# Kernel optimization log

Hardware: AMD Instinct MI355X
Metric: run time of the kernel (lower is better)

The kernel has to match this reference:

```python
import jax, jax.numpy as jnp
import numpy as np

B, C, H, W_SP = 1024, 256, 8, 8
HID = 512


def setup_inputs() -> dict:
    key = jax.random.key(0)
    ks = jax.random.split(key, 7)
    s_in = 1.0 / np.sqrt(C)
    s_hid = 1.0 / np.sqrt(HID)
    return {
        "anchor": jax.random.normal(ks[0], (B, C, H, W_SP), dtype=jnp.float32),
        "positive": jax.random.normal(ks[1], (B, C, H, W_SP), dtype=jnp.float32),
        "W1": jax.random.uniform(ks[2], (HID, C), minval=-s_in, maxval=s_in, dtype=jnp.float32),
        "b1": jax.random.uniform(ks[3], (HID,), minval=-s_in, maxval=s_in, dtype=jnp.float32),
        "W2": jax.random.uniform(ks[4], (C, HID), minval=-s_hid, maxval=s_hid, dtype=jnp.float32),
        "b2": jax.random.uniform(ks[5], (C,), minval=-s_hid, maxval=s_hid, dtype=jnp.float32),
        "Ww": jax.random.uniform(ks[6], (C, C), minval=-s_in, maxval=s_in, dtype=jnp.float32),
    }


def reference(anchor, positive, W1, b1, W2, b2, Ww):
    b, c, h, w = anchor.shape
    # Flatten spatial dims: [h*w, b, c] (equivalent to iterating y then x)
    a = jnp.transpose(anchor, (2, 3, 0, 1)).reshape(h * w, b, c)
    p = jnp.transpose(positive, (2, 3, 0, 1)).reshape(h * w, b, c)
    # anchor_xy = anchor_xy + MLP(anchor_xy); MLP = Linear->ReLU->Linear
    hidden = jax.nn.relu(jnp.einsum('pbc,hc->pbh', a, W1) + b1)
    a = a + jnp.einsum('pbh,ch->pbc', hidden, W2) + b2
    # pred_xy = W(anchor_xy), no bias
    pred = jnp.einsum('pbc,dc->pbd', a, Ww)
    # logits[p] = pred[p] @ positive[p].T : [h*w, b, b]
    logits = jnp.einsum('pbd,pkd->pbk', pred, p)
    logits = logits - jnp.max(logits, axis=2, keepdims=True)
    return logits  # [h*w, b, b], stacked version of the original python list
```

## Files before the change

kernel.cpp:

```cpp
#include <hip/hip_runtime.h>

typedef unsigned short u16;
typedef short bf16x8 __attribute__((ext_vector_type(8)));
typedef float f32x4 __attribute__((ext_vector_type(4)));

__device__ inline u16 f2bf(float f) {
  unsigned u = __float_as_uint(f);
  u += 0x7fff + ((u >> 16) & 1);
  return (u16)(u >> 16);
}

__device__ inline void gl_lds16(const u16* g, u16* l) {
  __builtin_amdgcn_global_load_lds((const __attribute__((address_space(1))) void*)g,
                                   (__attribute__((address_space(3))) void*)l, 16, 0, 0);
}

__global__ __launch_bounds__(256) void prep_weights(const float* __restrict__ Ww,
                                                    const float* __restrict__ W2,
                                                    const float* __restrict__ b2,
                                                    const float* __restrict__ W1,
                                                    u16* __restrict__ W2p,
                                                    float* __restrict__ b2p,
                                                    u16* __restrict__ W1b,
                                                    u16* __restrict__ Wwb) {
  int g = blockIdx.x * 256 + threadIdx.x;
  W1b[g] = f2bf(W1[g]);
  if (g < 65536) Wwb[g] = f2bf(Ww[g]);
  int d = g >> 9, h = g & 511;
  float s = 0.f;
  for (int c = 0; c < 256; c++) s += Ww[d * 256 + c] * W2[c * 512 + h];
  W2p[g] = f2bf(s);
  if (g < 256) {
    float t = 0.f;
    for (int c = 0; c < 256; c++) t += Ww[g * 256 + c] * b2[c];
    b2p[g] = t;
  }
}

__global__ __launch_bounds__(256) void transpose_cvt2(const float* __restrict__ ina,
                                                      const float* __restrict__ inp,
                                                      u16* __restrict__ outa,
                                                      u16* __restrict__ outp_) {
  __shared__ u16 T[64 * 256];
  const float* in = blockIdx.y ? inp : ina;
  u16* outp = blockIdx.y ? outp_ : outa;
  const int b = blockIdx.x;
  const int tid = threadIdx.x;
  const f32x4* in4 = (const f32x4*)in + (size_t)b * 4096;

  #pragma unroll
  for (int i = 0; i < 16; i++) {
    int local = i * 256 + tid;
    int c = local >> 4;
    int p4 = (local & 15) << 2;
    f32x4 v = __builtin_nontemporal_load(&in4[local]);
    int cc = c >> 3, co = c & 7;
    #pragma unroll
    for (int k = 0; k < 4; k++) {
      int p = p4 + k;
      int chunk = p * 32 + (cc ^ ((p >> 2) & 15));
      T[chunk * 8 + co] = f2bf(v[k]);
    }
  }
  __syncthreads();

  u16* ob = outp + (size_t)b * 256;
  #pragma unroll
  for (int j = 0; j < 8; j++) {
    int idx = j * 256 + tid;
    int row = idx >> 5;
    int col16 = idx & 31;
    int chunk = row * 32 + (col16 ^ ((row >> 2) & 15));
    bf16x8 vv = *(const bf16x8*)&T[chunk * 8];
    *(bf16x8*)&ob[((size_t)row << 18) + col16 * 8] = vv;
  }
}

__global__ __launch_bounds__(256, 3)
void gemm_bt(const u16* __restrict__ A1, const u16* __restrict__ B1, int K1len,
             const u16* __restrict__ A2, const u16* __restrict__ B2, int K2len,
             const float* __restrict__ bias, u16* __restrict__ C, int N, int relu,
             int lognbx) {
  __shared__ u16 As[128 * 64];
  __shared__ u16 Bs[128 * 64];
  const int tid = threadIdx.x;
  const int lane = tid & 63;
  const int wave = tid >> 6;
  const int wm = wave & 1;
  const int wn = wave >> 1;
  const int i_d = blockIdx.y * gridDim.x + blockIdx.x;
  const int xcd = i_d & 7;
  const int slot = i_d >> 3;
  const int bx = slot & ((1 << lognbx) - 1);
  const int by = xcd * (gridDim.y >> 3) + (slot >> lognbx);
  const int m0 = by * 128;
  const int n0 = bx * 128;
  const int q = lane >> 4;
  const int l15 = lane & 15;

  f32x4 acc[4][4];
  #pragma unroll
  for (int i = 0; i < 4; i++)
    #pragma unroll
    for (int j = 0; j < 4; j++) acc[i][j] = (f32x4)(0.0f);

  for (int seg = 0; seg < 2; seg++) {
    const u16* A = seg ? A2 : A1;
    const u16* B = seg ? B2 : B1;
    const int K = seg ? K2len : K1len;
    const int nkt = K >> 6;
    for (int kt = 0; kt < nkt; kt++) {
      #pragma unroll
      for (int c = 0; c < 4; c++) {
        int chunk = c * 256 + tid;
        int row = chunk >> 3;
        int cg = (chunk & 7) ^ (row & 7);
        gl_lds16(A + (size_t)(m0 + row) * K + kt * 64 + cg * 8, &As[chunk * 8]);
        gl_lds16(B + (size_t)(n0 + row) * K + kt * 64 + cg * 8, &Bs[chunk * 8]);
      }
      __syncthreads();
      #pragma unroll
      for (int ks = 0; ks < 2; ks++) {
        bf16x8 af[4], bfr[4];
        #pragma unroll
        for (int i = 0; i < 4; i++) {
          int row = wm * 64 + i * 16 + l15;
          af[i] = *(const bf16x8*)&As[row * 64 + (((ks * 4 + q) ^ (row & 7)) * 8)];
        }
        #pragma unroll
        for (int j = 0; j < 4; j++) {
          int row = wn * 64 + j * 16 + l15;
          bfr[j] = *(const bf16x8*)&Bs[row * 64 + (((ks * 4 + q) ^ (row & 7)) * 8)];
        }
        #pragma unroll
        for (int i = 0; i < 4; i++)
          #pragma unroll
          for (int j = 0; j < 4; j++)
            acc[i][j] = __builtin_amdgcn_mfma_f32_16x16x32_bf16(af[i], bfr[j], acc[i][j], 0, 0, 0);
      }
      __syncthreads();
    }
  }

  float bv[4];
  #pragma unroll
  for (int j = 0; j < 4; j++) bv[j] = bias[n0 + wn * 64 + j * 16 + l15];

  #pragma unroll
  for (int i = 0; i < 4; i++) {
    #pragma unroll
    for (int r = 0; r < 4; r++) {
      int row = m0 + wm * 64 + i * 16 + q * 4 + r;
      u16* crow = C + (size_t)row * N + n0 + wn * 64 + l15;
      #pragma unroll
      for (int j = 0; j < 4; j++) {
        float v = acc[i][j][r] + bv[j];
        if (relu) v = fmaxf(v, 0.0f);
        crow[j * 16] = f2bf(v);
      }
    }
  }
}

__global__ __launch_bounds__(512, 2)
void logits_k(const u16* __restrict__ pred, const u16* __restrict__ post,
              float* __restrict__ out) {
  __shared__ u16 As[64 * 256];
  __shared__ float pmax[8][64];
  const int tid = threadIdx.x;
  const int lane = tid & 63;
  const int wave = tid >> 6;
  const int q = lane >> 4;
  const int l15 = lane & 15;
  const int L = blockIdx.y * 16 + blockIdx.x;
  const int p = (L & 7) + ((L >> 7) << 3);
  const int m0 = ((L >> 3) & 15) * 64;
  const u16* Ap = pred + (((size_t)p * 1024 + m0) << 8);
  const u16* Bp = post + ((size_t)p << 18);

  #pragma unroll
  for (int c = 0; c < 4; c++) {
    int chunk = c * 512 + tid;
    int row = chunk >> 5;
    int cg = (chunk & 31) ^ (row & 7);
    gl_lds16(Ap + row * 256 + cg * 8, &As[chunk * 8]);
  }

  f32x4 acc[4][8];
  #pragma unroll
  for (int i = 0; i < 4; i++)
    #pragma unroll
    for (int j = 0; j < 8; j++) acc[i][j] = (f32x4)(0.0f);

  __syncthreads();

  const int nbase = wave * 128;
  #pragma unroll
  for (int kt = 0; kt < 8; kt++) {
    bf16x8 bfr[8];
    #pragma unroll
    for (int j = 0; j < 8; j++) {
      int n = nbase + j * 16 + l15;
      bfr[j] = *(const bf16x8*)&Bp[(size_t)n * 256 + kt * 32 + q * 8];
    }
    bf16x8 afr[4];
    #pragma unroll
    for (int i = 0; i < 4; i++) {
      int row = i * 16 + l15;
      afr[i] = *(const bf16x8*)&As[row * 256 + ((((kt << 2) + q) ^ (row & 7)) * 8)];
    }
    #pragma unroll
    for (int i = 0; i < 4; i++)
      #pragma unroll
      for (int j = 0; j < 8; j++)
        acc[i][j] = __builtin_amdgcn_mfma_f32_16x16x32_bf16(afr[i], bfr[j], acc[i][j], 0, 0, 0);
  }

  float rm[4][4];
  #pragma unroll
  for (int i = 0; i < 4; i++)
    #pragma unroll
    for (int r = 0; r < 4; r++) {
      float m = acc[i][0][r];
      #pragma unroll
      for (int j = 1; j < 8; j++) m = fmaxf(m, acc[i][j][r]);
      m = fmaxf(m, __shfl_xor(m, 1, 64));
      m = fmaxf(m, __shfl_xor(m, 2, 64));
      m = fmaxf(m, __shfl_xor(m, 4, 64));
      m = fmaxf(m, __shfl_xor(m, 8, 64));
      rm[i][r] = m;
    }
  if (l15 == 0) {
    #pragma unroll
    for (int i = 0; i < 4; i++)
      #pragma unroll
      for (int r = 0; r < 4; r++) pmax[wave][i * 16 + q * 4 + r] = rm[i][r];
  }
  __syncthreads();
  #pragma unroll
  for (int i = 0; i < 4; i++)
    #pragma unroll
    for (int r = 0; r < 4; r++) {
      int row = i * 16 + q * 4 + r;
      float m = pmax[0][row];
      #pragma unroll
      for (int w = 1; w < 8; w++) m = fmaxf(m, pmax[w][row]);
      rm[i][r] = m;
    }

  float* ob = out + ((size_t)p << 20) + (size_t)m0 * 1024 + nbase + l15;
  #pragma unroll
  for (int i = 0; i < 4; i++)
    #pragma unroll
    for (int r = 0; r < 4; r++) {
      float* orow = ob + (size_t)(i * 16 + q * 4 + r) * 1024;
      #pragma unroll
      for (int j = 0; j < 8; j++)
        __builtin_nontemporal_store(acc[i][j][r] - rm[i][r], &orow[j * 16]);
    }
}


extern "C" void kernel_launch(void* const* d_in, const int* in_sizes, int n_in,
                              void* d_out, int out_size, void* d_ws, size_t ws_size,
                              hipStream_t stream) {
  const float* anchor   = (const float*)d_in[0];
  const float* positive = (const float*)d_in[1];
  const float* W1       = (const float*)d_in[2];
  const float* b1       = (const float*)d_in[3];
  const float* W2       = (const float*)d_in[4];
  const float* b2       = (const float*)d_in[5];
  const float* Ww       = (const float*)d_in[6];
  float* out = (float*)d_out;
  char* ws = (char*)d_ws;

  u16*   A_t    = (u16*)(ws + 0x00000000);
  u16*   Pos_t  = (u16*)(ws + 0x02000000);
  u16*   hidden = (u16*)(ws + 0x04000000);
  u16*   pred   = (u16*)(ws + 0x08000000);
  u16*   W1b    = (u16*)(ws + 0x0A000000);
  u16*   Wwb    = (u16*)(ws + 0x0A100000);
  u16*   W2pb   = (u16*)(ws + 0x0A200000);
  float* b2p    = (float*)(ws + 0x0A300000);

  prep_weights<<<512, 256, 0, stream>>>(Ww, W2, b2, W1, W2pb, b2p, W1b, Wwb);
  transpose_cvt2<<<dim3(1024, 2), 256, 0, stream>>>(anchor, positive, A_t, Pos_t);

  gemm_bt<<<dim3(4, 512), 256, 0, stream>>>(A_t, W1b, 256, nullptr, nullptr, 0,
                                            b1, hidden, 512, 1, 2);
  gemm_bt<<<dim3(2, 512), 256, 0, stream>>>(A_t, Wwb, 256, hidden, W2pb, 512,
                                            b2p, pred, 256, 0, 1);
  logits_k<<<dim3(16, 64), 512, 0, stream>>>(pred, Pos_t, out);
}
```

Before: 522.0 us.

## Triple-buffer GEMM K-loop with async LDS loads and merge prep kernels

Rewrites the bf16 GEMM main loop to use a 3-stage ring of 32-wide K tiles loaded with global_load_lds, using partial vmcnt waits and one barrier per iteration so global loads overlap the MFMA work. The two K segments are flattened into one tile sequence so the pipeline carries across the segment boundary. Separately, weight preparation and input transpose/convert are merged into a single launch to remove one kernel launch and let the two run side by side. The smaller K tiles halve the work per barrier, and the hand-written waitcnt counts depend on the exact number of outstanding loads.

```diff
diff --git a/kernel.cpp b/kernel.cpp
--- a/kernel.cpp
+++ b/kernel.cpp
@@ -15,37 +15,37 @@
                                    (__attribute__((address_space(3))) void*)l, 16, 0, 0);
 }
 
-__global__ __launch_bounds__(256) void prep_weights(const float* __restrict__ Ww,
-                                                    const float* __restrict__ W2,
-                                                    const float* __restrict__ b2,
-                                                    const float* __restrict__ W1,
-                                                    u16* __restrict__ W2p,
-                                                    float* __restrict__ b2p,
-                                                    u16* __restrict__ W1b,
-                                                    u16* __restrict__ Wwb) {
-  int g = blockIdx.x * 256 + threadIdx.x;
-  W1b[g] = f2bf(W1[g]);
-  if (g < 65536) Wwb[g] = f2bf(Ww[g]);
-  int d = g >> 9, h = g & 511;
-  float s = 0.f;
-  for (int c = 0; c < 256; c++) s += Ww[d * 256 + c] * W2[c * 512 + h];
-  W2p[g] = f2bf(s);
-  if (g < 256) {
-    float t = 0.f;
-    for (int c = 0; c < 256; c++) t += Ww[g * 256 + c] * b2[c];
-    b2p[g] = t;
-  }
-}
-
-__global__ __launch_bounds__(256) void transpose_cvt2(const float* __restrict__ ina,
-                                                      const float* __restrict__ inp,
-                                                      u16* __restrict__ outa,
-                                                      u16* __restrict__ outp_) {
+__global__ __launch_bounds__(256) void prep_all(const float* __restrict__ anchor,
+                                                const float* __restrict__ positive,
+                                                u16* __restrict__ A_t, u16* __restrict__ Pos_t,
+                                                const float* __restrict__ Ww,
+                                                const float* __restrict__ W2,
+                                                const float* __restrict__ b2,
+                                                const float* __restrict__ W1,
+                                                u16* __restrict__ W2p, float* __restrict__ b2p,
+                                                u16* __restrict__ W1b, u16* __restrict__ Wwb) {
   __shared__ u16 T[64 * 256];
-  const float* in = blockIdx.y ? inp : ina;
-  u16* outp = blockIdx.y ? outp_ : outa;
-  const int b = blockIdx.x;
   const int tid = threadIdx.x;
+
+  if (blockIdx.x >= 2048) {
+    int g = (blockIdx.x - 2048) * 256 + tid;
+    W1b[g] = f2bf(W1[g]);
+    if (g < 65536) Wwb[g] = f2bf(Ww[g]);
+    int d = g >> 9, h = g & 511;
+    float s = 0.f;
+    for (int c = 0; c < 256; c++) s += Ww[d * 256 + c] * W2[c * 512 + h];
+    W2p[g] = f2bf(s);
+    if (g < 256) {
+      float t = 0.f;
+      for (int c = 0; c < 256; c++) t += Ww[g * 256 + c] * b2[c];
+      b2p[g] = t;
+    }
+    return;
+  }
+
+  const float* in = (blockIdx.x & 1024) ? positive : anchor;
+  u16* outp = (blockIdx.x & 1024) ? Pos_t : A_t;
+  const int b = blockIdx.x & 1023;
   const f32x4* in4 = (const f32x4*)in + (size_t)b * 4096;
 
   #pragma unroll
@@ -77,12 +77,12 @@
 }
 
 __global__ __launch_bounds__(256, 3)
-void gemm_bt(const u16* __restrict__ A1, const u16* __restrict__ B1, int K1len,
-             const u16* __restrict__ A2, const u16* __restrict__ B2, int K2len,
+void gemm_bt(const u16* __restrict__ A1, const u16* __restrict__ B1, int nkt1, int K1,
+             const u16* __restrict__ A2, const u16* __restrict__ B2, int nkt2, int K2,
              const float* __restrict__ bias, u16* __restrict__ C, int N, int relu,
              int lognbx) {
-  __shared__ u16 As[128 * 64];
-  __shared__ u16 Bs[128 * 64];
+  __shared__ u16 As[3][128 * 32];
+  __shared__ u16 Bs[3][128 * 32];
   const int tid = threadIdx.x;
   const int lane = tid & 63;
   const int wave = tid >> 6;
@@ -97,6 +97,21 @@
   const int n0 = bx * 128;
   const int q = lane >> 4;
   const int l15 = lane & 15;
+  const int nkt = nkt1 + nkt2;
+
+  auto stageF = [&](int kt, int buf) {
+    const u16* A; const u16* B; int K, k0;
+    if (kt < nkt1) { A = A1; B = B1; K = K1; k0 = kt << 5; }
+    else           { A = A2; B = B2; K = K2; k0 = (kt - nkt1) << 5; }
+    #pragma unroll
+    for (int c = 0; c < 2; c++) {
+      int chunk = c * 256 + tid;
+      int row = chunk >> 2;
+      int cg = (chunk & 3) ^ (row & 3);
+      gl_lds16(A + (size_t)(m0 + row) * K + k0 + cg * 8, &As[buf][chunk * 8]);
+      gl_lds16(B + (size_t)(n0 + row) * K + k0 + cg * 8, &Bs[buf][chunk * 8]);
+    }
+  };
 
   f32x4 acc[4][4];
   #pragma unroll
@@ -104,42 +119,38 @@
     #pragma unroll
     for (int j = 0; j < 4; j++) acc[i][j] = (f32x4)(0.0f);
 
-  for (int seg = 0; seg < 2; seg++) {
-    const u16* A = seg ? A2 : A1;
-    const u16* B = seg ? B2 : B1;
-    const int K = seg ? K2len : K1len;
-    const int nkt = K >> 6;
-    for (int kt = 0; kt < nkt; kt++) {
-      #pragma unroll
-      for (int c = 0; c < 4; c++) {
-        int chunk = c * 256 + tid;
-        int row = chunk >> 3;
-        int cg = (chunk & 7) ^ (row & 7);
-        gl_lds16(A + (size_t)(m0 + row) * K + kt * 64 + cg * 8, &As[chunk * 8]);
-        gl_lds16(B + (size_t)(n0 + row) * K + kt * 64 + cg * 8, &Bs[chunk * 8]);
-      }
-      __syncthreads();
-      #pragma unroll
-      for (int ks = 0; ks < 2; ks++) {
-        bf16x8 af[4], bfr[4];
-        #pragma unroll
-        for (int i = 0; i < 4; i++) {
-          int row = wm * 64 + i * 16 + l15;
-          af[i] = *(const bf16x8*)&As[row * 64 + (((ks * 4 + q) ^ (row & 7)) * 8)];
-        }
-        #pragma unroll
-        for (int j = 0; j < 4; j++) {
-          int row = wn * 64 + j * 16 + l15;
-          bfr[j] = *(const bf16x8*)&Bs[row * 64 + (((ks * 4 + q) ^ (row & 7)) * 8)];
-        }
-        #pragma unroll
-        for (int i = 0; i < 4; i++)
-          #pragma unroll
-          for (int j = 0; j < 4; j++)
-            acc[i][j] = __builtin_amdgcn_mfma_f32_16x16x32_bf16(af[i], bfr[j], acc[i][j], 0, 0, 0);
-      }
-      __syncthreads();
-    }
+  stageF(0, 0);
+  stageF(1, 1);
+  asm volatile("s_waitcnt vmcnt(4)" ::: "memory");
+  __builtin_amdgcn_s_barrier();
+
+  int cur = 0;
+  for (int kt = 0; kt < nkt; kt++) {
+    if (kt + 2 < nkt) stageF(kt + 2, cur == 0 ? 2 : cur - 1);
+
+    bf16x8 af[4], bfr[4];
+    #pragma unroll
+    for (int i = 0; i < 4; i++) {
+      int row = wm * 64 + i * 16 + l15;
+      af[i] = *(const bf16x8*)&As[cur][row * 32 + ((q ^ (row & 3)) * 8)];
+    }
+    #pragma unroll
+    for (int j = 0; j < 4; j++) {
+      int row = wn * 64 + j * 16 + l15;
+      bfr[j] = *(const bf16x8*)&Bs[cur][row * 32 + ((q ^ (row & 3)) * 8)];
+    }
+    #pragma unroll
+    for (int i = 0; i < 4; i++)
+      #pragma unroll
+      for (int j = 0; j < 4; j++)
+        acc[i][j] = __builtin_amdgcn_mfma_f32_16x16x32_bf16(af[i], bfr[j], acc[i][j], 0, 0, 0);
+
+    if (kt + 1 < nkt) {
+      if (kt + 2 < nkt) asm volatile("s_waitcnt vmcnt(4)" ::: "memory");
+      else              asm volatile("s_waitcnt vmcnt(0)" ::: "memory");
+      __builtin_amdgcn_s_barrier();
+    }
+    cur = (cur == 2) ? 0 : cur + 1;
   }
 
   float bv[4];
@@ -283,12 +294,12 @@
   u16*   W2pb   = (u16*)(ws + 0x0A200000);
   float* b2p    = (float*)(ws + 0x0A300000);
 
-  prep_weights<<<512, 256, 0, stream>>>(Ww, W2, b2, W1, W2pb, b2p, W1b, Wwb);
-  transpose_cvt2<<<dim3(1024, 2), 256, 0, stream>>>(anchor, positive, A_t, Pos_t);
-
-  gemm_bt<<<dim3(4, 512), 256, 0, stream>>>(A_t, W1b, 256, nullptr, nullptr, 0,
+  prep_all<<<2560, 256, 0, stream>>>(anchor, positive, A_t, Pos_t,
+                                     Ww, W2, b2, W1, W2pb, b2p, W1b, Wwb);
+
+  gemm_bt<<<dim3(4, 512), 256, 0, stream>>>(A_t, W1b, 8, 256, nullptr, nullptr, 0, 512,
                                             b1, hidden, 512, 1, 2);
-  gemm_bt<<<dim3(2, 512), 256, 0, stream>>>(A_t, Wwb, 256, hidden, W2pb, 512,
+  gemm_bt<<<dim3(2, 512), 256, 0, stream>>>(A_t, Wwb, 8, 256, hidden, W2pb, 16, 512,
                                             b2p, pred, 256, 0, 1);
   logits_k<<<dim3(16, 64), 512, 0, stream>>>(pred, Pos_t, out);
 }
```

Measured after the change: 530.1 us. No clear change (+1.6%).

## Fuse pred GEMM into logits kernel and merge prep kernels

Applied to the files above, without the earlier changes.

The weight-prep and transpose kernels become one launch with block-range dispatch. The second gemm_bt, which computed pred, is removed. Each logits block now computes its 64-row pred tile in LDS from A_t, hidden, Wwb and W2pb, then runs the logits GEMM. This drops the pred round trip through global memory and two launches, at the cost of a longer serial pred phase per block with B operands read straight from global memory, plus doubled LDS per block, which may reduce occupancy.

```diff
diff --git a/kernel.cpp b/kernel.cpp
--- a/kernel.cpp
+++ b/kernel.cpp
@@ -15,37 +15,37 @@
                                    (__attribute__((address_space(3))) void*)l, 16, 0, 0);
 }
 
-__global__ __launch_bounds__(256) void prep_weights(const float* __restrict__ Ww,
-                                                    const float* __restrict__ W2,
-                                                    const float* __restrict__ b2,
-                                                    const float* __restrict__ W1,
-                                                    u16* __restrict__ W2p,
-                                                    float* __restrict__ b2p,
-                                                    u16* __restrict__ W1b,
-                                                    u16* __restrict__ Wwb) {
-  int g = blockIdx.x * 256 + threadIdx.x;
-  W1b[g] = f2bf(W1[g]);
-  if (g < 65536) Wwb[g] = f2bf(Ww[g]);
-  int d = g >> 9, h = g & 511;
-  float s = 0.f;
-  for (int c = 0; c < 256; c++) s += Ww[d * 256 + c] * W2[c * 512 + h];
-  W2p[g] = f2bf(s);
-  if (g < 256) {
-    float t = 0.f;
-    for (int c = 0; c < 256; c++) t += Ww[g * 256 + c] * b2[c];
-    b2p[g] = t;
-  }
-}
-
-__global__ __launch_bounds__(256) void transpose_cvt2(const float* __restrict__ ina,
-                                                      const float* __restrict__ inp,
-                                                      u16* __restrict__ outa,
-                                                      u16* __restrict__ outp_) {
+__global__ __launch_bounds__(256) void prep_all(const float* __restrict__ anchor,
+                                                const float* __restrict__ positive,
+                                                u16* __restrict__ A_t, u16* __restrict__ Pos_t,
+                                                const float* __restrict__ Ww,
+                                                const float* __restrict__ W2,
+                                                const float* __restrict__ b2,
+                                                const float* __restrict__ W1,
+                                                u16* __restrict__ W2p, float* __restrict__ b2p,
+                                                u16* __restrict__ W1b, u16* __restrict__ Wwb) {
   __shared__ u16 T[64 * 256];
-  const float* in = blockIdx.y ? inp : ina;
-  u16* outp = blockIdx.y ? outp_ : outa;
-  const int b = blockIdx.x;
   const int tid = threadIdx.x;
+
+  if (blockIdx.x >= 2048) {
+    int g = (blockIdx.x - 2048) * 256 + tid;
+    W1b[g] = f2bf(W1[g]);
+    if (g < 65536) Wwb[g] = f2bf(Ww[g]);
+    int d = g >> 9, h = g & 511;
+    float s = 0.f;
+    for (int c = 0; c < 256; c++) s += Ww[d * 256 + c] * W2[c * 512 + h];
+    W2p[g] = f2bf(s);
+    if (g < 256) {
+      float t = 0.f;
+      for (int c = 0; c < 256; c++) t += Ww[g * 256 + c] * b2[c];
+      b2p[g] = t;
+    }
+    return;
+  }
+
+  const float* in = (blockIdx.x & 1024) ? positive : anchor;
+  u16* outp = (blockIdx.x & 1024) ? Pos_t : A_t;
+  const int b = blockIdx.x & 1023;
   const f32x4* in4 = (const f32x4*)in + (size_t)b * 4096;
 
   #pragma unroll
@@ -78,7 +78,6 @@
 
 __global__ __launch_bounds__(256, 3)
 void gemm_bt(const u16* __restrict__ A1, const u16* __restrict__ B1, int K1len,
-             const u16* __restrict__ A2, const u16* __restrict__ B2, int K2len,
              const float* __restrict__ bias, u16* __restrict__ C, int N, int relu,
              int lognbx) {
   __shared__ u16 As[128 * 64];
@@ -104,42 +103,37 @@
     #pragma unroll
     for (int j = 0; j < 4; j++) acc[i][j] = (f32x4)(0.0f);
 
-  for (int seg = 0; seg < 2; seg++) {
-    const u16* A = seg ? A2 : A1;
-    const u16* B = seg ? B2 : B1;
-    const int K = seg ? K2len : K1len;
-    const int nkt = K >> 6;
-    for (int kt = 0; kt < nkt; kt++) {
-      #pragma unroll
-      for (int c = 0; c < 4; c++) {
-        int chunk = c * 256 + tid;
-        int row = chunk >> 3;
-        int cg = (chunk & 7) ^ (row & 7);
-        gl_lds16(A + (size_t)(m0 + row) * K + kt * 64 + cg * 8, &As[chunk * 8]);
-        gl_lds16(B + (size_t)(n0 + row) * K + kt * 64 + cg * 8, &Bs[chunk * 8]);
+  const int nkt = K1len >> 6;
+  for (int kt = 0; kt < nkt; kt++) {
+    #pragma unroll
+    for (int c = 0; c < 4; c++) {
+      int chunk = c * 256 + tid;
+      int row = chunk >> 3;
+      int cg = (chunk & 7) ^ (row & 7);
+      gl_lds16(A1 + (size_t)(m0 + row) * K1len + kt * 64 + cg * 8, &As[chunk * 8]);
+      gl_lds16(B1 + (size_t)(n0 + row) * K1len + kt * 64 + cg * 8, &Bs[chunk * 8]);
+    }
+    __syncthreads();
+    #pragma unroll
+    for (int ks = 0; ks < 2; ks++) {
+      bf16x8 af[4], bfr[4];
+      #pragma unroll
+      for (int i = 0; i < 4; i++) {
+        int row = wm * 64 + i * 16 + l15;
+        af[i] = *(const bf16x8*)&As[row * 64 + (((ks * 4 + q) ^ (row & 7)) * 8)];
       }
-      __syncthreads();
-      #pragma unroll
-      for (int ks = 0; ks < 2; ks++) {
-        bf16x8 af[4], bfr[4];
+      #pragma unroll
+      for (int j = 0; j < 4; j++) {
+        int row = wn * 64 + j * 16 + l15;
+        bfr[j] = *(const bf16x8*)&Bs[row * 64 + (((ks * 4 + q) ^ (row & 7)) * 8)];
+      }
+      #pragma unroll
+      for (int i = 0; i < 4; i++)
         #pragma unroll
-        for (int i = 0; i < 4; i++) {
-          int row = wm * 64 + i * 16 + l15;
-          af[i] = *(const bf16x8*)&As[row * 64 + (((ks * 4 + q) ^ (row & 7)) * 8)];
-        }
-        #pragma unroll
-        for (int j = 0; j < 4; j++) {
-          int row = wn * 64 + j * 16 + l15;
-          bfr[j] = *(const bf16x8*)&Bs[row * 64 + (((ks * 4 + q) ^ (row & 7)) * 8)];
-        }
-        #pragma unroll
-        for (int i = 0; i < 4; i++)
-          #pragma unroll
-          for (int j = 0; j < 4; j++)
-            acc[i][j] = __builtin_amdgcn_mfma_f32_16x16x32_bf16(af[i], bfr[j], acc[i][j], 0, 0, 0);
-      }
-      __syncthreads();
-    }
+        for (int j = 0; j < 4; j++)
+          acc[i][j] = __builtin_amdgcn_mfma_f32_16x16x32_bf16(af[i], bfr[j], acc[i][j], 0, 0, 0);
+    }
+    __syncthreads();
   }
 
   float bv[4];
@@ -163,19 +157,24 @@
 }
 
 __global__ __launch_bounds__(512, 2)
-void logits_k(const u16* __restrict__ pred, const u16* __restrict__ post,
-              float* __restrict__ out) {
-  __shared__ u16 As[64 * 256];
+void pred_logits(const u16* __restrict__ A, const u16* __restrict__ hidden,
+                 const u16* __restrict__ Wwb, const u16* __restrict__ W2pb,
+                 const float* __restrict__ b2p, const u16* __restrict__ post,
+                 float* __restrict__ out) {
+  __shared__ u16 bufA[64 * 256];
+  __shared__ u16 bufB[64 * 256];
   __shared__ float pmax[8][64];
   const int tid = threadIdx.x;
   const int lane = tid & 63;
   const int wave = tid >> 6;
   const int q = lane >> 4;
   const int l15 = lane & 15;
-  const int L = blockIdx.y * 16 + blockIdx.x;
+  const int L = blockIdx.x;
   const int p = (L & 7) + ((L >> 7) << 3);
   const int m0 = ((L >> 3) & 15) * 64;
-  const u16* Ap = pred + (((size_t)p * 1024 + m0) << 8);
+  const size_t m0g = (size_t)p * 1024 + m0;
+  const u16* Ap = A + (m0g << 8);
+  const u16* Hp = hidden + (m0g << 9);
   const u16* Bp = post + ((size_t)p << 18);
 
   #pragma unroll
@@ -183,16 +182,82 @@
     int chunk = c * 512 + tid;
     int row = chunk >> 5;
     int cg = (chunk & 31) ^ (row & 7);
-    gl_lds16(Ap + row * 256 + cg * 8, &As[chunk * 8]);
-  }
+    gl_lds16(Ap + row * 256 + cg * 8, &bufA[chunk * 8]);
+    gl_lds16(Hp + (size_t)row * 512 + cg * 8, &bufB[chunk * 8]);
+  }
+
+  f32x4 accp[4][2];
+  #pragma unroll
+  for (int i = 0; i < 4; i++)
+    #pragma unroll
+    for (int j = 0; j < 2; j++) accp[i][j] = (f32x4)(0.0f);
+
+  const int nb = wave * 32;
+
+  __syncthreads();
+
+#define PSTEP(SRC, BG, BS, BOFF, KT)                                                     \
+  {                                                                                      \
+    bf16x8 bfr[2], afr[4];                                                               \
+    _Pragma("unroll")                                                                    \
+    for (int j = 0; j < 2; j++)                                                          \
+      bfr[j] = *(const bf16x8*)&(BG)[(size_t)(nb + j * 16 + l15) * (BS) + (BOFF) + (KT) * 32 + q * 8]; \
+    _Pragma("unroll")                                                                    \
+    for (int i = 0; i < 4; i++) {                                                        \
+      int row = i * 16 + l15;                                                            \
+      afr[i] = *(const bf16x8*)&(SRC)[row * 256 + ((((KT) * 4 + q) ^ (row & 7)) * 8)];   \
+    }                                                                                    \
+    _Pragma("unroll")                                                                    \
+    for (int i = 0; i < 4; i++)                                                          \
+      _Pragma("unroll")                                                                  \
+      for (int j = 0; j < 2; j++)                                                        \
+        accp[i][j] = __builtin_amdgcn_mfma_f32_16x16x32_bf16(afr[i], bfr[j], accp[i][j], 0, 0, 0); \
+  }
+
+  #pragma unroll
+  for (int kt = 0; kt < 8; kt++) PSTEP(bufA, Wwb, 256, 0, kt)
+  #pragma unroll
+  for (int kt = 0; kt < 8; kt++) PSTEP(bufB, W2pb, 512, 0, kt)
+
+  __syncthreads();
+
+  #pragma unroll
+  for (int c = 0; c < 4; c++) {
+    int chunk = c * 512 + tid;
+    int row = chunk >> 5;
+    int cg = (chunk & 31) ^ (row & 7);
+    gl_lds16(Hp + (size_t)row * 512 + 256 + cg * 8, &bufA[chunk * 8]);
+  }
+  __syncthreads();
+
+  #pragma unroll
+  for (int kt = 0; kt < 8; kt++) PSTEP(bufA, W2pb, 512, 256, kt)
+#undef PSTEP
+
+  {
+    float bv[2];
+    #pragma unroll
+    for (int j = 0; j < 2; j++) bv[j] = b2p[nb + j * 16 + l15];
+    #pragma unroll
+    for (int i = 0; i < 4; i++)
+      #pragma unroll
+      for (int r = 0; r < 4; r++) {
+        int row = i * 16 + q * 4 + r;
+        #pragma unroll
+        for (int j = 0; j < 2; j++) {
+          int col = nb + j * 16 + l15;
+          bufB[row * 256 + (((col >> 3) ^ (row & 7)) << 3) + (col & 7)] =
+              f2bf(accp[i][j][r] + bv[j]);
+        }
+      }
+  }
+  __syncthreads();
 
   f32x4 acc[4][8];
   #pragma unroll
   for (int i = 0; i < 4; i++)
     #pragma unroll
     for (int j = 0; j < 8; j++) acc[i][j] = (f32x4)(0.0f);
-
-  __syncthreads();
 
   const int nbase = wave * 128;
   #pragma unroll
@@ -207,7 +272,7 @@
     #pragma unroll
     for (int i = 0; i < 4; i++) {
       int row = i * 16 + l15;
-      afr[i] = *(const bf16x8*)&As[row * 256 + ((((kt << 2) + q) ^ (row & 7)) * 8)];
+      afr[i] = *(const bf16x8*)&bufB[row * 256 + ((((kt << 2) + q) ^ (row & 7)) * 8)];
     }
     #pragma unroll
     for (int i = 0; i < 4; i++)
@@ -277,18 +342,15 @@
   u16*   A_t    = (u16*)(ws + 0x00000000);
   u16*   Pos_t  = (u16*)(ws + 0x02000000);
   u16*   hidden = (u16*)(ws + 0x04000000);
-  u16*   pred   = (u16*)(ws + 0x08000000);
   u16*   W1b    = (u16*)(ws + 0x0A000000);
   u16*   Wwb    = (u16*)(ws + 0x0A100000);
   u16*   W2pb   = (u16*)(ws + 0x0A200000);
   float* b2p    = (float*)(ws + 0x0A300000);
 
-  prep_weights<<<512, 256, 0, stream>>>(Ww, W2, b2, W1, W2pb, b2p, W1b, Wwb);
-  transpose_cvt2<<<dim3(1024, 2), 256, 0, stream>>>(anchor, positive, A_t, Pos_t);
-
-  gemm_bt<<<dim3(4, 512), 256, 0, stream>>>(A_t, W1b, 256, nullptr, nullptr, 0,
-                                            b1, hidden, 512, 1, 2);
-  gemm_bt<<<dim3(2, 512), 256, 0, stream>>>(A_t, Wwb, 256, hidden, W2pb, 512,
-                                            b2p, pred, 256, 0, 1);
-  logits_k<<<dim3(16, 64), 512, 0, stream>>>(pred, Pos_t, out);
-}
+  prep_all<<<2560, 256, 0, stream>>>(anchor, positive, A_t, Pos_t,
+                                     Ww, W2, b2, W1, W2pb, b2p, W1b, Wwb);
+
+  gemm_bt<<<dim3(4, 512), 256, 0, stream>>>(A_t, W1b, 256, b1, hidden, 512, 1, 2);
+
+  pred_logits<<<1024, 512, 0, stream>>>(A_t, hidden, Wwb, W2pb, b2p, Pos_t, out);
+}
```

Result: slower. 546.4 us (+4.7%).
